# Performance work log

Hardware: AMD Instinct MI355X
Metric: run time of the kernel (lower is better)

The kernel has to match this reference:

```python
import jax, jax.numpy as jnp
import numpy as np

EMBED = 128   # embed_dims
NCAM = 6      # cameras per sample
FH, FW = 6, 12  # per-camera feature map size (same at every scale here)
THRESH = 0.01   # opacity threshold (GaussianRenderer.threshold)
SIZES = [25, 50, 100, 200]  # int(200 * 2**(s - 4 + 1)) for s in 0..3


def setup_inputs() -> dict:
    key = jax.random.key(0)
    ks = jax.random.split(key, 16)
    inp = {}
    for s in range(4):
        kf, km, ku, ko = ks[4 * s:4 * s + 4]
        inp[f"features{s}"] = jax.random.normal(kf, (NCAM, EMBED, FH, FW), dtype=jnp.float32)
        # means in the BEV range (-50, 50) meters
        inp[f"means{s}"] = jax.random.uniform(km, (NCAM, FH, FW, 3), minval=-50.0, maxval=50.0, dtype=jnp.float32)
        # PSD 3x3 uncertainty (covariance) per gaussian
        L = jax.random.normal(ku, (NCAM, FH, FW, 3, 3), dtype=jnp.float32)
        inp[f"uncert{s}"] = jnp.einsum('...ij,...kj->...ik', L, L) * 2.0 + jnp.eye(3, dtype=jnp.float32)
        inp[f"opac{s}"] = jax.random.uniform(ko, (NCAM, 1, FH, FW), dtype=jnp.float32)
    inp["b"] = 1
    inp["n"] = NCAM
    return inp


def _render_scale(feat, mean, unc, opac, H, W, b):
    # feat: [(b n), d, h, w]; mean: [(b n), h, w, 3]; unc: [(b n), h, w, 3, 3]; opac: [(b n), 1, h, w]
    bn, d, h, w = feat.shape
    N = (bn // b) * h * w
    f = feat.transpose(0, 2, 3, 1).reshape(b, N, d)          # b (n h w) d
    m = mean.reshape(b, N, 3)
    c9 = unc.reshape(b, N, 9)                                # flatten(-2,-1)
    # pack [xx, xy, xz, yy, yz, zz] then clamp(min=1)
    c6 = jnp.maximum(jnp.concatenate([c9[:, :, 0:3], c9[:, :, 4:6], c9[:, :, 8:9]], axis=-1), 1.0)
    o = opac.transpose(0, 2, 3, 1).reshape(b, N)

    # orthographic BEV projection: pix_row = -sh*y + H/2, pix_col = -sw*x + W/2
    sh = H / 100.0
    sw = W / 100.0
    pr = -sh * m[:, :, 1] + H / 2.0
    pc = -sw * m[:, :, 0] + W / 2.0

    # 2D covariance = J Sigma J^T with J = [[0,-sh,0],[-sw,0,0]]; +0.3 pixel dilation
    va = sh * sh * c6[:, :, 3] + 0.3   # row-row (from Sigma_yy)
    vb = sh * sw * c6[:, :, 1]         # row-col (from Sigma_xy)
    vc = sw * sw * c6[:, :, 0] + 0.3   # col-col (from Sigma_xx)
    det = va * vc - vb * vb

    rows = jnp.arange(H, dtype=feat.dtype)
    cols = jnp.arange(W, dtype=feat.dtype)
    dr = pr[:, :, None, None] - rows[None, None, :, None]    # [b,N,H,1]
    dc = pc[:, :, None, None] - cols[None, None, None, :]    # [b,N,1,W]

    power = (-0.5 * (vc[:, :, None, None] * dr * dr + va[:, :, None, None] * dc * dc)
             + vb[:, :, None, None] * dr * dc) / det[:, :, None, None]   # [b,N,H,W]

    keep = (o > THRESH) & (det > 0.0)                        # mask-gather expressed as alpha zeroing
    alpha = jnp.minimum(0.99, o[:, :, None, None] * jnp.exp(jnp.minimum(power, 0.0)))
    alpha = jnp.where(keep[:, :, None, None] & (power <= 0.0) & (alpha >= 1.0 / 255.0), alpha, 0.0)

    # front-to-back alpha compositing in gaussian order (depth is identically 0 in BEV)
    A = alpha.reshape(b, N, H * W)
    T = jnp.cumprod(1.0 - A, axis=1)
    T_excl = jnp.concatenate([jnp.ones_like(T[:, :1]), T[:, :-1]], axis=1)
    out = jnp.einsum('bnp,bnd->bdp', A * T_excl, f).reshape(b, d, H, W)  # bg color is zeros

    num_g = (o > THRESH).astype(feat.dtype).sum(1).mean()
    return out, num_g


def reference(features0, features1, features2, features3,
              means0, means1, means2, means3,
              uncert0, uncert1, uncert2, uncert3,
              opac0, opac1, opac2, opac3, b, n):
    feats = [features0, features1, features2, features3]
    means = [means0, means1, means2, means3]
    uncs = [uncert0, uncert1, uncert2, uncert3]
    ops = [opac0, opac1, opac2, opac3]
    outs = []
    num_gaussians = jnp.float32(0.0)
    for s in range(4):
        o, g = _render_scale(feats[s], means[s], uncs[s], ops[s], SIZES[s], SIZES[s], b)
        outs.append(o)
        num_gaussians = num_gaussians + g
    return (outs[0], outs[1], outs[2], outs[3], num_gaussians)
```

## Files before the change

kernel.cpp:

```cpp
#include <hip/hip_runtime.h>

#define NCAM   6
#define FHW    72
#define EMBED  128
#define NG     432
#define THRESH 0.01f
#define AMIN   (1.0f/255.0f)
#define NTILES 891
#define TC     432

struct Args {
    const float* feat[4];
    const float* mean[4];
    const float* unc[4];
    const float* opac[4];
};

__device__ __forceinline__ void tile_decode(int g, int& s, int& H, int& band, int& chunk)
{
    int tb;
    if (g < 14)       { s = 0; H = 25;  tb = g;       chunk = tb & 1;  band = tb >> 1; }
    else if (g < 66)  { s = 1; H = 50;  tb = g - 14;  chunk = tb & 3;  band = tb >> 2; }
    else if (g < 241) { s = 2; H = 100; tb = g - 66;  band = tb / 7;   chunk = tb - band * 7; }
    else              { s = 3; H = 200; tb = g - 241; band = tb / 13;  chunk = tb - band * 13; }
}

__global__ __launch_bounds__(256) void prep(Args a, float* __restrict__ ft,
                                            int* __restrict__ tlen,
                                            float4* __restrict__ p4a,
                                            float4* __restrict__ p4b,
                                            float* __restrict__ out)
{
    int b = blockIdx.x, t = threadIdx.x;
    if (b < NTILES) {
        __shared__ int s_cnt[8];
        int g = b;
        int s, H, band, chunk;
        tile_decode(g, s, H, band, chunk);
        int lane = t & 63, wv = t >> 6;
        float sh = H * 0.01f;
        float r0f = (float)(band * 4), r1f = (float)min(band * 4 + 3, H - 1);
        float c0f = (float)(chunk * 16), c1f = (float)min(chunk * 16 + 15, H - 1);
        const float* mean = a.mean[s];
        const float* unc  = a.unc[s];
        const float* opac = a.opac[s];

        bool v_act[2]; int v_rnk[2];
        float v_pr[2], v_pc[2], v_qa[2], v_qb[2], v_qc[2], v_ok[2];
        #pragma unroll
        for (int pp = 0; pp < 2; pp++) {
            int j = pp * 256 + t;
            bool act = false;
            float pr = 0.f, pc = 0.f, qa = 0.f, qb = 0.f, qc = 0.f, ok = 0.f;
            if (j < NG) {
                float m0 = mean[j*3+0], m1 = mean[j*3+1];
                float u00 = fmaxf(unc[j*9+0], 1.f);
                float u01 = fmaxf(unc[j*9+1], 1.f);
                float u11 = fmaxf(unc[j*9+4], 1.f);
                float op = opac[j];
                pr = -sh*m1 + H*0.5f;
                pc = -sh*m0 + H*0.5f;
                float va = sh*sh*u11 + 0.3f;
                float vb = sh*sh*u01;
                float vc = sh*sh*u00 + 0.3f;
                float det = va*vc - vb*vb;
                if (op > THRESH && det > 0.f) {
                    float inv = 1.f/det;
                    qa = 0.5f*vc*inv;
                    qc = 0.5f*va*inv;
                    qb = vb*inv;
                    ok = op;
                    float thr = __logf(255.f*op);
                    float Rr = sqrtf(2.f*va*thr) + 1e-2f;
                    float Rc = sqrtf(2.f*vc*thr) + 1e-2f;
                    act = (pr >= r0f-Rr) && (pr <= r1f+Rr) &&
                          (pc >= c0f-Rc) && (pc <= c1f+Rc);
                }
            }
            unsigned long long m = __ballot(act);
            v_act[pp] = act;
            v_rnk[pp] = __popcll(m & ((1ull << lane) - 1ull));
            v_pr[pp]=pr; v_pc[pp]=pc; v_qa[pp]=qa; v_qb[pp]=qb; v_qc[pp]=qc; v_ok[pp]=ok;
            if (lane == 0) s_cnt[pp*4 + wv] = __popcll(m);
        }
        __syncthreads();
        int c8[8];
        #pragma unroll
        for (int i = 0; i < 8; i++) c8[i] = s_cnt[i];
        int len = 0;
        #pragma unroll
        for (int i = 0; i < 8; i++) len += c8[i];
        #pragma unroll
        for (int pp = 0; pp < 2; pp++) {
            int slot = pp*4 + wv;
            int pre = 0;
            #pragma unroll
            for (int i = 0; i < 8; i++) pre += (i < slot) ? c8[i] : 0;
            if (v_act[pp]) {
                int idx = g*TC + pre + v_rnk[pp];
                int j = pp * 256 + t;
                unsigned off = (unsigned)((s*NG + j) * EMBED);
                p4a[idx] = make_float4(v_pr[pp], v_pc[pp], v_qa[pp], v_qb[pp]);
                p4b[idx] = make_float4(v_qc[pp], v_ok[pp], __uint_as_float(off), 0.f);
            }
        }
        if (t == 0) tlen[g] = len;
    } else if (b < NTILES + 24) {
        __shared__ float l[EMBED * 73];
        int sc = b - NTILES;
        int s = sc / NCAM, cam = sc - s * NCAM;
        const float* src = a.feat[s] + cam * (EMBED * FHW);
        for (int i = t; i < EMBED * FHW; i += 256) {
            int d = i / FHW, hw = i - d * FHW;
            l[d * 73 + hw] = src[i];
        }
        __syncthreads();
        float* dst = ft + (s * NG + cam * FHW) * EMBED;
        for (int e = t; e < EMBED * FHW; e += 256) {
            int hw = e >> 7, d = e & 127;
            dst[hw * EMBED + d] = l[d * 73 + hw];
        }
    } else {
        __shared__ float red[256];
        float c = 0.f;
        for (int s = 0; s < 4; s++)
            for (int i = t; i < NG; i += 256)
                c += (a.opac[s][i] > THRESH) ? 1.f : 0.f;
        red[t] = c;
        __syncthreads();
        for (int st = 128; st > 0; st >>= 1) {
            if (t < st) red[t] += red[t + st];
            __syncthreads();
        }
        if (t == 0) out[6800000] = red[0];
    }
}

__global__ __launch_bounds__(256) void render(const float* __restrict__ ft,
                                              const int* __restrict__ tlen,
                                              const float4* __restrict__ p4a,
                                              const float4* __restrict__ p4b,
                                              float* __restrict__ out)
{
    __shared__ float s_T[4][64];
    __shared__ float s_part[3][64][33];

    int bb = blockIdx.x, t = threadIdx.x;
    int g = bb >> 2, chq = bb & 3;
    int s, H, band, chunk;
    tile_decode(g, s, H, band, chunk);
    int P = H * H;
    float* o = out + ((s == 0) ? 0 : (s == 1) ? 80000 : (s == 2) ? 400000 : 1680000);
    int lane = t & 63;
    int wv = __builtin_amdgcn_readfirstlane(t >> 6);
    int ch0 = chq * 32;
    int len = tlen[g];
    int qlen = (len + 3) >> 2;
    int k0 = wv * qlen, k1 = min(k0 + qlen, len);
    int base = g * TC;
    int row = band*4 + (lane >> 4), col = chunk*16 + (lane & 15);
    float frow = (float)row, fcol = (float)col;

    float acc[32];
    #pragma unroll
    for (int i = 0; i < 32; i++) acc[i] = 0.f;
    float T = 1.f;

    for (int k = k0; k < k1; k++) {
        float4 A = p4a[base + k];
        float4 B = p4b[base + k];
        unsigned off = __builtin_amdgcn_readfirstlane(__float_as_uint(B.z));
        const float* fr = ft + off + ch0;
        float dr = A.x - frow, dc = A.y - fcol;
        float pw = A.w*dr*dc - A.z*dr*dr - B.x*dc*dc;
        float aL = 0.f;
        if (pw <= 0.f) {
            aL = fminf(B.y * __expf(pw), 0.99f);
            aL = (aL >= AMIN) ? aL : 0.f;
        }
        float w = aL * T;
        T *= (1.f - aL);
        #pragma unroll
        for (int i = 0; i < 32; i += 4) {
            float4 f = *reinterpret_cast<const float4*>(fr + i);
            acc[i]   += w * f.x; acc[i+1] += w * f.y;
            acc[i+2] += w * f.z; acc[i+3] += w * f.w;
        }
    }

    s_T[wv][lane] = T;
    __syncthreads();
    if (wv > 0) {
        float pref = s_T[0][lane];
        if (wv > 1) pref *= s_T[1][lane];
        if (wv > 2) pref *= s_T[2][lane];
        #pragma unroll
        for (int i = 0; i < 32; i++)
            s_part[wv-1][lane][i] = acc[i] * pref;
    }
    __syncthreads();
    if (wv == 0 && row < H && col < H) {
        int pp = row * H + col;
        #pragma unroll
        for (int i = 0; i < 32; i++) {
            float v = acc[i] + s_part[0][lane][i] + s_part[1][lane][i]
                             + s_part[2][lane][i];
            o[(ch0 + i) * P + pp] = v;
        }
    }
}

extern "C" void kernel_launch(void* const* d_in, const int* in_sizes, int n_in,
                              void* d_out, int out_size, void* d_ws, size_t ws_size,
                              hipStream_t stream)
{
    Args a;
    for (int s = 0; s < 4; s++) {
        a.feat[s] = (const float*)d_in[4 * s + 0];
        a.mean[s] = (const float*)d_in[4 * s + 1];
        a.unc[s]  = (const float*)d_in[4 * s + 2];
        a.opac[s] = (const float*)d_in[4 * s + 3];
    }
    float* ws = (float*)d_ws;
    float*  ft   = ws;
    int*    tlen = (int*)(ws + 221184);
    float4* p4a  = (float4*)(ws + 222080);
    float4* p4b  = p4a + NTILES * TC;

    prep<<<NTILES + 24 + 1, 256, 0, stream>>>(a, ft, tlen, p4a, p4b, (float*)d_out);
    render<<<NTILES * 4, 256, 0, stream>>>(ft, tlen, p4a, p4b, (float*)d_out);
}
```

Before: 27.07 us.

## Fuse per-tile gaussian culling into render kernel using shared-memory lists

Per-tile culling and compaction of gaussians moves from the prep kernel into the render kernel. Each render block now rebuilds its tile's active list in LDS instead of reading it from global workspace buffers, so prep shrinks to the feature transpose and count blocks. The render loop also software-pipelines the feature loads, fetching the next gaussian's feature row while accumulating the current one. In exchange, culling work is repeated four times per tile (once per channel-quarter block), and the larger LDS footprint may lower occupancy.

```diff
diff --git a/kernel.cpp b/kernel.cpp
--- a/kernel.cpp
+++ b/kernel.cpp
@@ -26,89 +26,12 @@
 }
 
 __global__ __launch_bounds__(256) void prep(Args a, float* __restrict__ ft,
-                                            int* __restrict__ tlen,
-                                            float4* __restrict__ p4a,
-                                            float4* __restrict__ p4b,
                                             float* __restrict__ out)
 {
     int b = blockIdx.x, t = threadIdx.x;
-    if (b < NTILES) {
-        __shared__ int s_cnt[8];
-        int g = b;
-        int s, H, band, chunk;
-        tile_decode(g, s, H, band, chunk);
-        int lane = t & 63, wv = t >> 6;
-        float sh = H * 0.01f;
-        float r0f = (float)(band * 4), r1f = (float)min(band * 4 + 3, H - 1);
-        float c0f = (float)(chunk * 16), c1f = (float)min(chunk * 16 + 15, H - 1);
-        const float* mean = a.mean[s];
-        const float* unc  = a.unc[s];
-        const float* opac = a.opac[s];
-
-        bool v_act[2]; int v_rnk[2];
-        float v_pr[2], v_pc[2], v_qa[2], v_qb[2], v_qc[2], v_ok[2];
-        #pragma unroll
-        for (int pp = 0; pp < 2; pp++) {
-            int j = pp * 256 + t;
-            bool act = false;
-            float pr = 0.f, pc = 0.f, qa = 0.f, qb = 0.f, qc = 0.f, ok = 0.f;
-            if (j < NG) {
-                float m0 = mean[j*3+0], m1 = mean[j*3+1];
-                float u00 = fmaxf(unc[j*9+0], 1.f);
-                float u01 = fmaxf(unc[j*9+1], 1.f);
-                float u11 = fmaxf(unc[j*9+4], 1.f);
-                float op = opac[j];
-                pr = -sh*m1 + H*0.5f;
-                pc = -sh*m0 + H*0.5f;
-                float va = sh*sh*u11 + 0.3f;
-                float vb = sh*sh*u01;
-                float vc = sh*sh*u00 + 0.3f;
-                float det = va*vc - vb*vb;
-                if (op > THRESH && det > 0.f) {
-                    float inv = 1.f/det;
-                    qa = 0.5f*vc*inv;
-                    qc = 0.5f*va*inv;
-                    qb = vb*inv;
-                    ok = op;
-                    float thr = __logf(255.f*op);
-                    float Rr = sqrtf(2.f*va*thr) + 1e-2f;
-                    float Rc = sqrtf(2.f*vc*thr) + 1e-2f;
-                    act = (pr >= r0f-Rr) && (pr <= r1f+Rr) &&
-                          (pc >= c0f-Rc) && (pc <= c1f+Rc);
-                }
-            }
-            unsigned long long m = __ballot(act);
-            v_act[pp] = act;
-            v_rnk[pp] = __popcll(m & ((1ull << lane) - 1ull));
-            v_pr[pp]=pr; v_pc[pp]=pc; v_qa[pp]=qa; v_qb[pp]=qb; v_qc[pp]=qc; v_ok[pp]=ok;
-            if (lane == 0) s_cnt[pp*4 + wv] = __popcll(m);
-        }
-        __syncthreads();
-        int c8[8];
-        #pragma unroll
-        for (int i = 0; i < 8; i++) c8[i] = s_cnt[i];
-        int len = 0;
-        #pragma unroll
-        for (int i = 0; i < 8; i++) len += c8[i];
-        #pragma unroll
-        for (int pp = 0; pp < 2; pp++) {
-            int slot = pp*4 + wv;
-            int pre = 0;
-            #pragma unroll
-            for (int i = 0; i < 8; i++) pre += (i < slot) ? c8[i] : 0;
-            if (v_act[pp]) {
-                int idx = g*TC + pre + v_rnk[pp];
-                int j = pp * 256 + t;
-                unsigned off = (unsigned)((s*NG + j) * EMBED);
-                p4a[idx] = make_float4(v_pr[pp], v_pc[pp], v_qa[pp], v_qb[pp]);
-                p4b[idx] = make_float4(v_qc[pp], v_ok[pp], __uint_as_float(off), 0.f);
-            }
-        }
-        if (t == 0) tlen[g] = len;
-    } else if (b < NTILES + 24) {
+    if (b < 24) {
         __shared__ float l[EMBED * 73];
-        int sc = b - NTILES;
-        int s = sc / NCAM, cam = sc - s * NCAM;
+        int s = b / NCAM, cam = b - s * NCAM;
         const float* src = a.feat[s] + cam * (EMBED * FHW);
         for (int i = t; i < EMBED * FHW; i += 256) {
             int d = i / FHW, hw = i - d * FHW;
@@ -136,14 +59,13 @@
     }
 }
 
-__global__ __launch_bounds__(256) void render(const float* __restrict__ ft,
-                                              const int* __restrict__ tlen,
-                                              const float4* __restrict__ p4a,
-                                              const float4* __restrict__ p4b,
+__global__ __launch_bounds__(256) void render(Args a, const float* __restrict__ ft,
                                               float* __restrict__ out)
 {
-    __shared__ float s_T[4][64];
-    __shared__ float s_part[3][64][33];
+    __shared__ __align__(16) char smem[26368];
+    __shared__ int s_cnt[8];
+    float4* e0 = (float4*)smem;
+    float4* e1 = (float4*)(smem + 6912);
 
     int bb = blockIdx.x, t = threadIdx.x;
     int g = bb >> 2, chq = bb & 3;
@@ -153,11 +75,77 @@
     float* o = out + ((s == 0) ? 0 : (s == 1) ? 80000 : (s == 2) ? 400000 : 1680000);
     int lane = t & 63;
     int wv = __builtin_amdgcn_readfirstlane(t >> 6);
+    float sh = H * 0.01f;
+    float r0f = (float)(band * 4), r1f = (float)min(band * 4 + 3, H - 1);
+    float c0f = (float)(chunk * 16), c1f = (float)min(chunk * 16 + 15, H - 1);
+    const float* mean = a.mean[s];
+    const float* unc  = a.unc[s];
+    const float* opac = a.opac[s];
+
+    bool v_act[2]; int v_rnk[2];
+    float v_pr[2], v_pc[2], v_qa[2], v_qb[2], v_qc[2], v_ok[2];
+    #pragma unroll
+    for (int pp = 0; pp < 2; pp++) {
+        int j = pp * 256 + t;
+        bool act = false;
+        float pr = 0.f, pc = 0.f, qa = 0.f, qb = 0.f, qc = 0.f, ok = 0.f;
+        if (j < NG) {
+            float m0 = mean[j*3+0], m1 = mean[j*3+1];
+            float u00 = fmaxf(unc[j*9+0], 1.f);
+            float u01 = fmaxf(unc[j*9+1], 1.f);
+            float u11 = fmaxf(unc[j*9+4], 1.f);
+            float op = opac[j];
+            pr = -sh*m1 + H*0.5f;
+            pc = -sh*m0 + H*0.5f;
+            float va = sh*sh*u11 + 0.3f;
+            float vb = sh*sh*u01;
+            float vc = sh*sh*u00 + 0.3f;
+            float det = va*vc - vb*vb;
+            if (op > THRESH && det > 0.f) {
+                float inv = 1.f/det;
+                qa = 0.5f*vc*inv;
+                qc = 0.5f*va*inv;
+                qb = vb*inv;
+                ok = op;
+                float thr = __logf(255.f*op);
+                float Rr = sqrtf(2.f*va*thr) + 1e-2f;
+                float Rc = sqrtf(2.f*vc*thr) + 1e-2f;
+                act = (pr >= r0f-Rr) && (pr <= r1f+Rr) &&
+                      (pc >= c0f-Rc) && (pc <= c1f+Rc);
+            }
+        }
+        unsigned long long m = __ballot(act);
+        v_act[pp] = act;
+        v_rnk[pp] = __popcll(m & ((1ull << lane) - 1ull));
+        v_pr[pp]=pr; v_pc[pp]=pc; v_qa[pp]=qa; v_qb[pp]=qb; v_qc[pp]=qc; v_ok[pp]=ok;
+        if (lane == 0) s_cnt[pp*4 + wv] = __popcll(m);
+    }
+    __syncthreads();
+    int c8[8];
+    #pragma unroll
+    for (int i = 0; i < 8; i++) c8[i] = s_cnt[i];
+    int len = 0;
+    #pragma unroll
+    for (int i = 0; i < 8; i++) len += c8[i];
+    #pragma unroll
+    for (int pp = 0; pp < 2; pp++) {
+        int slot = pp*4 + wv;
+        int pre = 0;
+        #pragma unroll
+        for (int i = 0; i < 8; i++) pre += (i < slot) ? c8[i] : 0;
+        if (v_act[pp]) {
+            int idx = pre + v_rnk[pp];
+            int j = pp * 256 + t;
+            unsigned off = (unsigned)((s*NG + j) * EMBED);
+            e0[idx] = make_float4(v_pr[pp], v_pc[pp], v_qa[pp], v_qb[pp]);
+            e1[idx] = make_float4(v_qc[pp], v_ok[pp], __uint_as_float(off), 0.f);
+        }
+    }
+    __syncthreads();
+
+    int qlen = (len + 3) >> 2;
+    int k0 = wv * qlen, k1v = min(k0 + qlen, len);
     int ch0 = chq * 32;
-    int len = tlen[g];
-    int qlen = (len + 3) >> 2;
-    int k0 = wv * qlen, k1 = min(k0 + qlen, len);
-    int base = g * TC;
     int row = band*4 + (lane >> 4), col = chunk*16 + (lane & 15);
     float frow = (float)row, fcol = (float)col;
 
@@ -166,45 +154,64 @@
     for (int i = 0; i < 32; i++) acc[i] = 0.f;
     float T = 1.f;
 
-    for (int k = k0; k < k1; k++) {
-        float4 A = p4a[base + k];
-        float4 B = p4b[base + k];
-        unsigned off = __builtin_amdgcn_readfirstlane(__float_as_uint(B.z));
-        const float* fr = ft + off + ch0;
-        float dr = A.x - frow, dc = A.y - fcol;
-        float pw = A.w*dr*dc - A.z*dr*dr - B.x*dc*dc;
-        float aL = 0.f;
-        if (pw <= 0.f) {
-            aL = fminf(B.y * __expf(pw), 0.99f);
-            aL = (aL >= AMIN) ? aL : 0.f;
-        }
-        float w = aL * T;
-        T *= (1.f - aL);
-        #pragma unroll
-        for (int i = 0; i < 32; i += 4) {
-            float4 f = *reinterpret_cast<const float4*>(fr + i);
-            acc[i]   += w * f.x; acc[i+1] += w * f.y;
-            acc[i+2] += w * f.z; acc[i+3] += w * f.w;
-        }
-    }
-
-    s_T[wv][lane] = T;
+    if (k0 < k1v) {
+        float4 A = e0[k0], Bv = e1[k0];
+        unsigned off0 = __builtin_amdgcn_readfirstlane(__float_as_uint(Bv.z));
+        const float* fr = ft + off0 + ch0;
+        float4 f[8];
+        #pragma unroll
+        for (int i = 0; i < 8; i++)
+            f[i] = *reinterpret_cast<const float4*>(fr + i * 4);
+
+        for (int k = k0; k < k1v; k++) {
+            int kn = (k + 1 < k1v) ? k + 1 : k;
+            float4 An = e0[kn], Bn = e1[kn];
+            float dr = A.x - frow, dc = A.y - fcol;
+            float pw = A.w*dr*dc - A.z*dr*dr - Bv.x*dc*dc;
+            float aL = 0.f;
+            if (pw <= 0.f) {
+                aL = fminf(Bv.y * __expf(pw), 0.99f);
+                aL = (aL >= AMIN) ? aL : 0.f;
+            }
+            float w = aL * T;
+            T *= (1.f - aL);
+            #pragma unroll
+            for (int i = 0; i < 8; i++) {
+                acc[i*4]   += w * f[i].x;
+                acc[i*4+1] += w * f[i].y;
+                acc[i*4+2] += w * f[i].z;
+                acc[i*4+3] += w * f[i].w;
+            }
+            unsigned offn = __builtin_amdgcn_readfirstlane(__float_as_uint(Bn.z));
+            const float* frn = ft + offn + ch0;
+            #pragma unroll
+            for (int i = 0; i < 8; i++)
+                f[i] = *reinterpret_cast<const float4*>(frn + i * 4);
+            A = An; Bv = Bn;
+        }
+    }
+
+    __syncthreads();
+    float* s_T    = (float*)smem;
+    float* s_part = (float*)(smem + 1024);
+    s_T[wv * 64 + lane] = T;
     __syncthreads();
     if (wv > 0) {
-        float pref = s_T[0][lane];
-        if (wv > 1) pref *= s_T[1][lane];
-        if (wv > 2) pref *= s_T[2][lane];
+        float pref = s_T[lane];
+        if (wv > 1) pref *= s_T[64 + lane];
+        if (wv > 2) pref *= s_T[128 + lane];
         #pragma unroll
         for (int i = 0; i < 32; i++)
-            s_part[wv-1][lane][i] = acc[i] * pref;
+            s_part[(wv - 1) * 2112 + lane * 33 + i] = acc[i] * pref;
     }
     __syncthreads();
     if (wv == 0 && row < H && col < H) {
         int pp = row * H + col;
         #pragma unroll
         for (int i = 0; i < 32; i++) {
-            float v = acc[i] + s_part[0][lane][i] + s_part[1][lane][i]
-                             + s_part[2][lane][i];
+            float v = acc[i] + s_part[lane * 33 + i]
+                             + s_part[2112 + lane * 33 + i]
+                             + s_part[4224 + lane * 33 + i];
             o[(ch0 + i) * P + pp] = v;
         }
     }
@@ -222,11 +229,8 @@
         a.opac[s] = (const float*)d_in[4 * s + 3];
     }
     float* ws = (float*)d_ws;
-    float*  ft   = ws;
-    int*    tlen = (int*)(ws + 221184);
-    float4* p4a  = (float4*)(ws + 222080);
-    float4* p4b  = p4a + NTILES * TC;
-
-    prep<<<NTILES + 24 + 1, 256, 0, stream>>>(a, ft, tlen, p4a, p4b, (float*)d_out);
-    render<<<NTILES * 4, 256, 0, stream>>>(ft, tlen, p4a, p4b, (float*)d_out);
-}
+    float* ft = ws;
+
+    prep<<<25, 256, 0, stream>>>(a, ft, (float*)d_out);
+    render<<<NTILES * 4, 256, 0, stream>>>(a, ft, (float*)d_out);
+}
```

New measurement: 29.91 us. +10.5%, slower.

## Broadcast per-lane feature loads via readlane, prefetch gaussians, skip inactive splats

Applied to the files above, without the earlier changes.

The render loop changes so each lane loads one feature channel of the current gaussian with a single coalesced load. The values are broadcast across the wave with readlane instead of every lane issuing redundant float4 loads. Gaussian parameters and features are software-prefetched two and one steps ahead, and the feature accumulation is skipped when no pixel in the wave gets nonzero weight. Tiles of scales 1–3 now process 64 channels per block (two blocks per tile) to halve the number of parameter passes. This raises register pressure and the scalar readlane count, and the 32-channel path reads slightly past the feature buffer end.

```diff
diff --git a/kernel.cpp b/kernel.cpp
--- a/kernel.cpp
+++ b/kernel.cpp
@@ -136,55 +136,62 @@
     }
 }
 
-__global__ __launch_bounds__(256) void render(const float* __restrict__ ft,
-                                              const int* __restrict__ tlen,
-                                              const float4* __restrict__ p4a,
-                                              const float4* __restrict__ p4b,
-                                              float* __restrict__ out)
-{
-    __shared__ float s_T[4][64];
-    __shared__ float s_part[3][64][33];
-
-    int bb = blockIdx.x, t = threadIdx.x;
-    int g = bb >> 2, chq = bb & 3;
+template<int NCH>
+__device__ __forceinline__ void render_body(
+    int g, int ch0, int t,
+    const float* __restrict__ ft, const int* __restrict__ tlen,
+    const float4* __restrict__ p4a, const float4* __restrict__ p4b,
+    float* __restrict__ out, float (*s_T)[64], float (*s_part)[64][65])
+{
     int s, H, band, chunk;
     tile_decode(g, s, H, band, chunk);
     int P = H * H;
     float* o = out + ((s == 0) ? 0 : (s == 1) ? 80000 : (s == 2) ? 400000 : 1680000);
     int lane = t & 63;
     int wv = __builtin_amdgcn_readfirstlane(t >> 6);
-    int ch0 = chq * 32;
     int len = tlen[g];
-    int qlen = (len + 3) >> 2;
-    int k0 = wv * qlen, k1 = min(k0 + qlen, len);
+    int ql = (len + 3) >> 2;
+    int k0 = min(wv * ql, len), k1 = min(k0 + ql, len);
     int base = g * TC;
     int row = band*4 + (lane >> 4), col = chunk*16 + (lane & 15);
     float frow = (float)row, fcol = (float)col;
 
-    float acc[32];
+    float acc[NCH];
     #pragma unroll
-    for (int i = 0; i < 32; i++) acc[i] = 0.f;
+    for (int c = 0; c < NCH; c++) acc[c] = 0.f;
     float T = 1.f;
 
-    for (int k = k0; k < k1; k++) {
-        float4 A = p4a[base + k];
-        float4 B = p4b[base + k];
-        unsigned off = __builtin_amdgcn_readfirstlane(__float_as_uint(B.z));
-        const float* fr = ft + off + ch0;
-        float dr = A.x - frow, dc = A.y - fcol;
-        float pw = A.w*dr*dc - A.z*dr*dr - B.x*dc*dc;
-        float aL = 0.f;
-        if (pw <= 0.f) {
-            aL = fminf(B.y * __expf(pw), 0.99f);
-            aL = (aL >= AMIN) ? aL : 0.f;
-        }
-        float w = aL * T;
-        T *= (1.f - aL);
-        #pragma unroll
-        for (int i = 0; i < 32; i += 4) {
-            float4 f = *reinterpret_cast<const float4*>(fr + i);
-            acc[i]   += w * f.x; acc[i+1] += w * f.y;
-            acc[i+2] += w * f.z; acc[i+3] += w * f.w;
+    if (k0 < k1) {
+        float4 A = p4a[base + k0], B = p4b[base + k0];
+        float fv = ft[__builtin_amdgcn_readfirstlane((int)__float_as_uint(B.z)) + ch0 + lane];
+        float4 A1, B1;
+        {
+            int kn = min(k0 + 1, k1 - 1);
+            A1 = p4a[base + kn]; B1 = p4b[base + kn];
+        }
+        for (int k = k0; k < k1; k++) {
+            int k2 = min(k + 2, k1 - 1);
+            float4 A2 = p4a[base + k2], B2 = p4b[base + k2];
+            float fv1 = ft[__builtin_amdgcn_readfirstlane((int)__float_as_uint(B1.z))
+                           + ch0 + lane];
+            float dr = A.x - frow, dc = A.y - fcol;
+            float pw = A.w*dr*dc - A.z*dr*dr - B.x*dc*dc;
+            float aL = 0.f;
+            if (pw <= 0.f) {
+                aL = fminf(B.y * __expf(pw), 0.99f);
+                aL = (aL >= AMIN) ? aL : 0.f;
+            }
+            float w = aL * T;
+            T *= (1.f - aL);
+            if (__any(w > 0.f)) {
+                #pragma unroll
+                for (int c = 0; c < NCH; c++) {
+                    float fc = __uint_as_float(
+                        (unsigned)__builtin_amdgcn_readlane((int)__float_as_uint(fv), c));
+                    acc[c] += w * fc;
+                }
+            }
+            A = A1; B = B1; A1 = A2; B1 = B2; fv = fv1;
         }
     }
 
@@ -195,18 +202,42 @@
         if (wv > 1) pref *= s_T[1][lane];
         if (wv > 2) pref *= s_T[2][lane];
         #pragma unroll
-        for (int i = 0; i < 32; i++)
-            s_part[wv-1][lane][i] = acc[i] * pref;
+        for (int c = 0; c < NCH; c++)
+            s_part[wv-1][c][lane] = acc[c] * pref;
     }
     __syncthreads();
     if (wv == 0 && row < H && col < H) {
         int pp = row * H + col;
         #pragma unroll
-        for (int i = 0; i < 32; i++) {
-            float v = acc[i] + s_part[0][lane][i] + s_part[1][lane][i]
-                             + s_part[2][lane][i];
-            o[(ch0 + i) * P + pp] = v;
-        }
+        for (int c = 0; c < NCH; c++) {
+            float v = acc[c] + s_part[0][c][lane] + s_part[1][c][lane]
+                             + s_part[2][c][lane];
+            o[(ch0 + c) * P + pp] = v;
+        }
+    }
+}
+
+__global__ __launch_bounds__(256) void render(const float* __restrict__ ft,
+                                              const int* __restrict__ tlen,
+                                              const float4* __restrict__ p4a,
+                                              const float4* __restrict__ p4b,
+                                              float* __restrict__ out)
+{
+    __shared__ float s_T[4][64];
+    __shared__ float s_part[3][64][65];
+
+    int bb = blockIdx.x, t = threadIdx.x;
+    if (bb < 56) {
+        render_body<32>(bb >> 2, (bb & 3) * 32, t, ft, tlen, p4a, p4b, out, s_T, s_part);
+    } else if (bb < 160) {
+        int i = bb - 56;
+        render_body<64>(14 + (i >> 1), (i & 1) * 64, t, ft, tlen, p4a, p4b, out, s_T, s_part);
+    } else if (bb < 510) {
+        int i = bb - 160;
+        render_body<64>(66 + (i >> 1), (i & 1) * 64, t, ft, tlen, p4a, p4b, out, s_T, s_part);
+    } else {
+        int i = bb - 510;
+        render_body<64>(241 + (i >> 1), (i & 1) * 64, t, ft, tlen, p4a, p4b, out, s_T, s_part);
     }
 }
 
@@ -228,5 +259,5 @@
     float4* p4b  = p4a + NTILES * TC;
 
     prep<<<NTILES + 24 + 1, 256, 0, stream>>>(a, ft, tlen, p4a, p4b, (float*)d_out);
-    render<<<NTILES * 4, 256, 0, stream>>>(ft, tlen, p4a, p4b, (float*)d_out);
-}
+    render<<<1810, 256, 0, stream>>>(ft, tlen, p4a, p4b, (float*)d_out);
+}
```

Result: slower. 31.95 us (+18.0%).

## Skip zero-weight feature loads, terminate early, and split render work per scale

Applied to the files above, without the earlier changes.

Per-gaussian parameters move from two separate arrays into one interleaved array. The render loop now loads feature rows only when some lane in the wave has a nonzero weight, and it stops once every lane's transmittance falls below 1e-5. Only the 66 small-scale tiles keep the 4-way depth split with the shared-memory merge. For the larger scales, one block per tile has each wave take a 32-channel quarter over the full gaussian list, so no merge is needed. Together this cuts feature-load traffic and the block count, at the cost of serial per-wave loops on long lists and a small approximation from early termination.

```diff
diff --git a/kernel.cpp b/kernel.cpp
--- a/kernel.cpp
+++ b/kernel.cpp
@@ -27,8 +27,7 @@
 
 __global__ __launch_bounds__(256) void prep(Args a, float* __restrict__ ft,
                                             int* __restrict__ tlen,
-                                            float4* __restrict__ p4a,
-                                            float4* __restrict__ p4b,
+                                            float4* __restrict__ p8,
                                             float* __restrict__ out)
 {
     int b = blockIdx.x, t = threadIdx.x;
@@ -100,8 +99,8 @@
                 int idx = g*TC + pre + v_rnk[pp];
                 int j = pp * 256 + t;
                 unsigned off = (unsigned)((s*NG + j) * EMBED);
-                p4a[idx] = make_float4(v_pr[pp], v_pc[pp], v_qa[pp], v_qb[pp]);
-                p4b[idx] = make_float4(v_qc[pp], v_ok[pp], __uint_as_float(off), 0.f);
+                p8[idx*2 + 0] = make_float4(v_pr[pp], v_pc[pp], v_qa[pp], v_qb[pp]);
+                p8[idx*2 + 1] = make_float4(v_qc[pp], v_ok[pp], __uint_as_float(off), 0.f);
             }
         }
         if (t == 0) tlen[g] = len;
@@ -138,26 +137,33 @@
 
 __global__ __launch_bounds__(256) void render(const float* __restrict__ ft,
                                               const int* __restrict__ tlen,
-                                              const float4* __restrict__ p4a,
-                                              const float4* __restrict__ p4b,
+                                              const float4* __restrict__ p8,
                                               float* __restrict__ out)
 {
     __shared__ float s_T[4][64];
     __shared__ float s_part[3][64][33];
 
     int bb = blockIdx.x, t = threadIdx.x;
-    int g = bb >> 2, chq = bb & 3;
+    int lane = t & 63;
+    int wv = __builtin_amdgcn_readfirstlane(t >> 6);
+    int g, chq;
+    bool ksplit;
+    if (bb < 264) { g = bb >> 2; chq = bb & 3; ksplit = true; }
+    else          { g = 66 + (bb - 264); chq = wv; ksplit = false; }
+
     int s, H, band, chunk;
     tile_decode(g, s, H, band, chunk);
     int P = H * H;
     float* o = out + ((s == 0) ? 0 : (s == 1) ? 80000 : (s == 2) ? 400000 : 1680000);
-    int lane = t & 63;
-    int wv = __builtin_amdgcn_readfirstlane(t >> 6);
+    int len = tlen[g];
+    int k0 = 0, k1 = len;
+    if (ksplit) {
+        int ql = (len + 3) >> 2;
+        k0 = min(wv * ql, len);
+        k1 = min(k0 + ql, len);
+    }
     int ch0 = chq * 32;
-    int len = tlen[g];
-    int qlen = (len + 3) >> 2;
-    int k0 = wv * qlen, k1 = min(k0 + qlen, len);
-    int base = g * TC;
+    const float4* pb = p8 + (size_t)(g * TC) * 2;
     int row = band*4 + (lane >> 4), col = chunk*16 + (lane & 15);
     float frow = (float)row, fcol = (float)col;
 
@@ -167,10 +173,8 @@
     float T = 1.f;
 
     for (int k = k0; k < k1; k++) {
-        float4 A = p4a[base + k];
-        float4 B = p4b[base + k];
-        unsigned off = __builtin_amdgcn_readfirstlane(__float_as_uint(B.z));
-        const float* fr = ft + off + ch0;
+        float4 A = pb[2*k];
+        float4 B = pb[2*k + 1];
         float dr = A.x - frow, dc = A.y - fcol;
         float pw = A.w*dr*dc - A.z*dr*dr - B.x*dc*dc;
         float aL = 0.f;
@@ -180,12 +184,29 @@
         }
         float w = aL * T;
         T *= (1.f - aL);
-        #pragma unroll
-        for (int i = 0; i < 32; i += 4) {
-            float4 f = *reinterpret_cast<const float4*>(fr + i);
-            acc[i]   += w * f.x; acc[i+1] += w * f.y;
-            acc[i+2] += w * f.z; acc[i+3] += w * f.w;
-        }
+        if (__any(w > 0.f)) {
+            unsigned off = __builtin_amdgcn_readfirstlane(__float_as_uint(B.z));
+            const float* fr = ft + off + ch0;
+            #pragma unroll
+            for (int i = 0; i < 32; i += 4) {
+                float4 f = *reinterpret_cast<const float4*>(fr + i);
+                acc[i]   += w * f.x; acc[i+1] += w * f.y;
+                acc[i+2] += w * f.z; acc[i+3] += w * f.w;
+            }
+        }
+        if (__all(T < 1e-5f)) break;
+    }
+
+    bool inb = (row < H) && (col < H);
+    int pp = row * H + col;
+
+    if (!ksplit) {
+        if (inb) {
+            #pragma unroll
+            for (int i = 0; i < 32; i++)
+                o[(ch0 + i) * P + pp] = acc[i];
+        }
+        return;
     }
 
     s_T[wv][lane] = T;
@@ -199,8 +220,7 @@
             s_part[wv-1][lane][i] = acc[i] * pref;
     }
     __syncthreads();
-    if (wv == 0 && row < H && col < H) {
-        int pp = row * H + col;
+    if (wv == 0 && inb) {
         #pragma unroll
         for (int i = 0; i < 32; i++) {
             float v = acc[i] + s_part[0][lane][i] + s_part[1][lane][i]
@@ -224,9 +244,8 @@
     float* ws = (float*)d_ws;
     float*  ft   = ws;
     int*    tlen = (int*)(ws + 221184);
-    float4* p4a  = (float4*)(ws + 222080);
-    float4* p4b  = p4a + NTILES * TC;
-
-    prep<<<NTILES + 24 + 1, 256, 0, stream>>>(a, ft, tlen, p4a, p4b, (float*)d_out);
-    render<<<NTILES * 4, 256, 0, stream>>>(ft, tlen, p4a, p4b, (float*)d_out);
-}
+    float4* p8   = (float4*)(ws + 222080);
+
+    prep<<<NTILES + 24 + 1, 256, 0, stream>>>(a, ft, tlen, p8, (float*)d_out);
+    render<<<264 + 825, 256, 0, stream>>>(ft, tlen, p8, (float*)d_out);
+}
```

Result: slower. 32.38 us (+19.6%).
